# Kernel optimization log

Hardware: AMD Instinct MI355X
Metric: run time of the kernel (lower is better)

The kernel has to match this reference:

```python
import jax, jax.numpy as jnp
import numpy as np

N_NODES = 50000
N_EDGES = 200000
D = 128          # in_channels == num_hidden_channels == out_channels (set_out_input_dim_equal)
H = 4            # num_att_heads
C = D            # out_channels per head
R = 8            # num_relations
NEG_SLOPE = 0.2  # GATv2 leaky_relu slope


def gelu(x):
    # torch nn.GELU default = exact erf form
    return jax.nn.gelu(x, approximate=False)


def setup_inputs() -> dict:
    key = jax.random.key(0)
    ks = jax.random.split(key, 8)
    embs = jax.random.normal(ks[0], (N_NODES, D), dtype=jnp.float32)
    edge_index = jax.random.randint(ks[1], (2, N_EDGES), 0, N_NODES)
    edge_type = jax.random.randint(ks[2], (N_EDGES,), 0, R)
    # glorot for relation matrices [R, 2D, D]
    lim = float(np.sqrt(6.0 / (2 * D + D)))
    rel_matrices = jax.random.uniform(ks[3], (R, 2 * D, D), jnp.float32, -lim, lim)
    # GATv2Conv lin_l (== lin_r, share_weights=True): D -> H*C, with bias
    lim_l = float(np.sqrt(6.0 / (D + H * C)))
    W_l = jax.random.uniform(ks[4], (D, H * C), jnp.float32, -lim_l, lim_l)
    b_l = jnp.zeros((H * C,), jnp.float32)
    # lin_edge: edge_dim=D -> H*C, no bias
    W_e = jax.random.uniform(ks[5], (D, H * C), jnp.float32, -lim_l, lim_l)
    # attention vector att: [H, C]
    lim_a = float(np.sqrt(6.0 / C))
    att = jax.random.uniform(ks[6], (H, C), jnp.float32, -lim_a, lim_a)
    # final bias (concat=True -> size H*C)
    bias = jnp.zeros((H * C,), jnp.float32)
    return {"embs": embs, "edge_index": edge_index, "edge_type": edge_type,
            "rel_matrices": rel_matrices, "W_l": W_l, "b_l": b_l,
            "W_e": W_e, "att": att, "bias": bias, "batch_size": 1024}


def reference(embs, edge_index, edge_type, rel_matrices, W_l, b_l, W_e, att, bias, batch_size):
    src = edge_index[0]  # x_j / message source
    trg = edge_index[1]  # x_i / aggregation target

    # ---- create_edge_attrs: per-edge relation-specific bmm + GELU ----
    e_emb = jnp.concatenate([embs[src], embs[trg]], axis=1)  # [E, 2D]
    acc = jnp.zeros((e_emb.shape[0], D), e_emb.dtype)
    for r in range(R):  # fixed small relation set; avoids [E,2D,D] materialization
        acc = acc + jnp.where((edge_type == r)[:, None], e_emb @ rel_matrices[r], 0.0)
    edge_attr = gelu(acc)  # [E, D]

    # ---- GATv2Conv (share_weights=True, add_self_loops=False, concat) ----
    x = (embs @ W_l + b_l).reshape(N_NODES, H, C)  # lin_l == lin_r
    x_j = x[src]                                    # [E, H, C]
    x_i = x[trg]                                    # [E, H, C]
    e_p = (edge_attr @ W_e).reshape(-1, H, C)       # [E, H, C]

    z = jax.nn.leaky_relu(x_i + x_j + e_p, NEG_SLOPE)
    logits = jnp.einsum('ehc,hc->eh', z, att)       # [E, H]

    # edge softmax over incoming edges per target node (numerically stable)
    m = jax.ops.segment_max(logits, trg, num_segments=N_NODES)
    m = jnp.where(jnp.isfinite(m), m, 0.0)
    ex = jnp.exp(logits - m[trg])
    s = jax.ops.segment_sum(ex, trg, num_segments=N_NODES)
    alpha = ex / jnp.maximum(s[trg], 1e-16)         # [E, H]

    out = jax.ops.segment_sum(x_j * alpha[..., None], trg, num_segments=N_NODES)
    out = out.reshape(N_NODES, H * C) + bias        # concat heads
    # single (last) layer: no trailing dropout / GELU
    return out
```

## Files before the change

kernel.cpp:

```cpp
#include <hip/hip_runtime.h>
#include <math.h>

#define D_DIM 128
#define TWO_D 256
#define HC    512
#define NH    4
#define RNUM  8
#define BM    128

#define M_CNT  0
#define M_OFF  8
#define M_BLK  17
#define M_CUR  26
#define M_CUR2 34

typedef __attribute__((ext_vector_type(8))) short v8s;
typedef __attribute__((ext_vector_type(4))) float v4f;
typedef __attribute__((ext_vector_type(8))) unsigned short us8;

#define MFMA(a,b,c) __builtin_amdgcn_mfma_f32_16x16x32_bf16((a),(b),(c),0,0,0)

__device__ __forceinline__ float bf2f(unsigned short v){
    return __uint_as_float(((unsigned)v) << 16);
}
__device__ __forceinline__ unsigned short f2bf(float f){
    unsigned u = __float_as_uint(f);
    u += 0x7fffu + ((u >> 16) & 1u);
    return (unsigned short)(u >> 16);
}

__device__ __forceinline__ v8s frag_ld(const unsigned short* buf, int r, int chunk){
    return *(const v8s*)(buf + r * 64 + ((chunk ^ (r & 7)) << 3));
}

template<typename RowFn>
__device__ __forceinline__ void stage_gl(unsigned short* lds, RowFn rowp, int col0, int tid){
    const int lane = tid & 63;
    const int w = tid >> 6;
    #pragma unroll
    for (int i = 0; i < 4; i++){
        const int k = w * 4 + i;
        const int o = k * 1024 + lane * 16;
        const int rr = o >> 7;
        const int cp = (o & 127) >> 4;
        const int cg = cp ^ (rr & 7);
        const unsigned short* src = rowp(rr) + col0 + cg * 8;
        unsigned short* dst = lds + k * 512;
        __builtin_amdgcn_global_load_lds((const __attribute__((address_space(1))) void*)src,
                                         (__attribute__((address_space(3))) void*)dst,
                                         16, 0, 0);
    }
}

__global__ void k_prep(const float* __restrict__ embs, const float* __restrict__ rel,
                       const float* __restrict__ W_e, const float* __restrict__ W_l,
                       unsigned short* __restrict__ embs_bf, unsigned short* __restrict__ rel_t,
                       unsigned short* __restrict__ W_e_t, unsigned short* __restrict__ W_l_t,
                       int* __restrict__ meta, int* __restrict__ tcnt, int* __restrict__ tcur,
                       int N){
    const long T0 = (long)N * D_DIM;
    const long T1 = T0 + (long)RNUM * D_DIM * TWO_D;
    const long T2 = T1 + (long)HC * D_DIM;
    const long T3 = T2 + (long)HC * D_DIM;
    const long stride = (long)gridDim.x * blockDim.x;
    const long gid = (long)blockIdx.x * blockDim.x + threadIdx.x;

    for (long i = gid; i < N; i += stride){ tcnt[i] = 0; tcur[i] = 0; }
    if (gid < RNUM) meta[M_CNT + gid] = 0;

    const long NE8 = T0 / 8;
    for (long i = gid; i < NE8; i += stride){
        const float4* p = (const float4*)(embs + i * 8);
        float4 a = p[0], b = p[1];
        us8 o;
        o[0]=f2bf(a.x); o[1]=f2bf(a.y); o[2]=f2bf(a.z); o[3]=f2bf(a.w);
        o[4]=f2bf(b.x); o[5]=f2bf(b.y); o[6]=f2bf(b.z); o[7]=f2bf(b.w);
        *(us8*)(embs_bf + i * 8) = o;
    }
    for (long i = T0 + gid; i < T3; i += stride){
        if (i < T1){
            long j = i - T0;
            int r = (int)(j >> 15);
            int rem = (int)(j & 32767);
            int n = rem >> 8, k = rem & 255;
            rel_t[j] = f2bf(rel[(long)r * 32768 + (long)k * D_DIM + n]);
        } else if (i < T2){
            long j = i - T1;
            int n = (int)(j >> 7), k = (int)(j & 127);
            W_e_t[j] = f2bf(W_e[(long)k * HC + n]);
        } else {
            long j = i - T2;
            int n = (int)(j >> 7), k = (int)(j & 127);
            W_l_t[j] = f2bf(W_l[(long)k * HC + n]);
        }
    }
}

__global__ void k_count(const int* __restrict__ etype, const int* __restrict__ trg,
                        int* __restrict__ meta, int* __restrict__ tcnt, int E){
    __shared__ int h[RNUM];
    int tid = threadIdx.x;
    if (tid < RNUM) h[tid] = 0;
    __syncthreads();
    int e = blockIdx.x * 256 + tid;
    if (e < E){
        atomicAdd(&h[etype[e]], 1);
        atomicAdd(&tcnt[trg[e]], 1);
    }
    __syncthreads();
    if (tid < RNUM) atomicAdd(&meta[M_CNT + tid], h[tid]);
}

__global__ __launch_bounds__(256) void k_bsum(const int* __restrict__ tcnt,
                                              int* __restrict__ bsum,
                                              int* __restrict__ meta, int N){
    __shared__ int red[256];
    int tid = threadIdx.x;
    int i = blockIdx.x * 256 + tid;
    red[tid] = (i < N) ? tcnt[i] : 0;
    __syncthreads();
    for (int off = 128; off > 0; off >>= 1){
        if (tid < off) red[tid] += red[tid + off];
        __syncthreads();
    }
    if (tid == 0) bsum[blockIdx.x] = red[0];
    if (blockIdx.x == 0 && tid == 0){
        int offv = 0, blkv = 0;
        meta[M_OFF] = 0; meta[M_BLK] = 0;
        for (int r2 = 0; r2 < RNUM; r2++){
            int c = meta[M_CNT + r2];
            offv += c; blkv += (c + BM - 1) / BM;
            meta[M_OFF + r2 + 1] = offv;
            meta[M_BLK + r2 + 1] = blkv;
            meta[M_CUR + r2] = 0;
            meta[M_CUR2 + r2] = 0;
        }
    }
}

__global__ __launch_bounds__(256) void k_cscan(const int* __restrict__ tcnt,
                                               const int* __restrict__ bsum,
                                               int* __restrict__ rowptr, int N, int NB){
    __shared__ int pre[256];
    __shared__ int sOff;
    int tid = threadIdx.x;
    int b = blockIdx.x;

    int s = 0;
    for (int j = tid; j < b; j += 256) s += bsum[j];
    pre[tid] = s;
    __syncthreads();
    for (int off = 128; off > 0; off >>= 1){
        if (tid < off) pre[tid] += pre[tid + off];
        __syncthreads();
    }
    if (tid == 0) sOff = pre[0];
    __syncthreads();
    const int base = sOff;
    __syncthreads();

    int i = b * 256 + tid;
    int v = (i < N) ? tcnt[i] : 0;
    pre[tid] = v;
    __syncthreads();
    for (int off = 1; off < 256; off <<= 1){
        int t = (tid >= off) ? pre[tid - off] : 0;
        __syncthreads();
        pre[tid] += t;
        __syncthreads();
    }
    if (i < N) rowptr[i] = base + pre[tid] - v;
    if (i == N) rowptr[N] = base + pre[tid];
    if (b == NB - 1 && (b + 1) * 256 == N && tid == 255)
        rowptr[N] = base + pre[255];
}

__global__ void k_scatter2(const int* __restrict__ etype, const int* __restrict__ trg,
                           const int* __restrict__ src,
                           const int* __restrict__ rowptr, int* __restrict__ tcur,
                           int* __restrict__ srcp, int* __restrict__ trgp,
                           int* __restrict__ etypep, int E){
    int e = blockIdx.x * 256 + threadIdx.x;
    if (e < E){
        int t = trg[e];
        int pos = rowptr[t] + atomicAdd(&tcur[t], 1);
        srcp[pos] = src[e];
        trgp[pos] = t;
        etypep[pos] = etype[e];
    }
}

__global__ void k_rscatter(const int* __restrict__ etypep, int* __restrict__ meta,
                           int* __restrict__ perm, int E){
    __shared__ int lcnt[RNUM], lbase[RNUM];
    int tid = threadIdx.x;
    if (tid < RNUM) lcnt[tid] = 0;
    __syncthreads();
    int p = blockIdx.x * 256 + tid;
    int r = 0, rank = 0;
    if (p < E){ r = etypep[p]; rank = atomicAdd(&lcnt[r], 1); }
    __syncthreads();
    if (tid < RNUM) lbase[tid] = atomicAdd(&meta[M_CUR2 + tid], lcnt[tid]);
    __syncthreads();
    if (p < E) perm[meta[M_OFF + r] + lbase[r] + rank] = p;
}

#define ZP 132

__global__ __launch_bounds__(256, 4) void k_x_mfma(
    const unsigned short* __restrict__ embs_bf, const unsigned short* __restrict__ W_l_t,
    const float* __restrict__ b_l, unsigned short* __restrict__ x_bf, int N)
{
    __shared__ __align__(16) char smem[64 * ZP * 4];
    unsigned short* Ab = (unsigned short*)smem;
    unsigned short* Bb = (unsigned short*)(smem + 16384);
    float* zb = (float*)smem;

    const int tid = threadIdx.x;
    const int n0 = blockIdx.x * BM;
    const int cg = blockIdx.y;
    const int cnt = min(BM, N - n0);
    const int w = tid >> 6, lane = tid & 63, m = lane & 15, q = lane >> 4;

    v4f acc[2][8];
    #pragma unroll
    for (int i = 0; i < 2; i++)
        #pragma unroll
        for (int j = 0; j < 8; j++) acc[i][j] = 0.f;

    #pragma unroll
    for (int ch = 0; ch < 2; ch++){
        __syncthreads();
        stage_gl(Ab, [&](int rr){ return embs_bf + (long)min(n0 + rr, N - 1) * D_DIM; },
                 ch * 64, tid);
        stage_gl(Bb, [&](int rr){ return W_l_t + (long)(cg * BM + rr) * D_DIM; },
                 ch * 64, tid);
        __syncthreads();
        #pragma unroll
        for (int ks = 0; ks < 2; ks++){
            v8s af[2], bf[8];
            #pragma unroll
            for (int rt = 0; rt < 2; rt++) af[rt] = frag_ld(Ab, w*32 + rt*16 + m, ks*4 + q);
            #pragma unroll
            for (int ct = 0; ct < 8; ct++) bf[ct] = frag_ld(Bb, ct*16 + m, ks*4 + q);
            #pragma unroll
            for (int rt = 0; rt < 2; rt++)
                #pragma unroll
                for (int ct = 0; ct < 8; ct++)
                    acc[rt][ct] = MFMA(af[rt], bf[ct], acc[rt][ct]);
        }
    }
    __syncthreads();

    for (int pp = 0; pp < 2; pp++){
        if ((w >> 1) == pp){
            int wr = (w & 1) * 32;
            #pragma unroll
            for (int rt = 0; rt < 2; rt++)
                #pragma unroll
                for (int ct = 0; ct < 8; ct++)
                    #pragma unroll
                    for (int g = 0; g < 4; g++)
                        zb[(wr + rt*16 + q*4 + g) * ZP + ct*16 + m] = acc[rt][ct][g];
        }
        __syncthreads();
        int rl = tid >> 2, pq = tid & 3;
        int row = pp * 64 + rl;
        if (row < cnt){
            const float* zp = zb + rl * ZP + pq * 32;
            const float* blp = b_l + cg * BM + pq * 32;
            long dst = (long)(n0 + row) * HC + cg * BM + pq * 32;
            #pragma unroll
            for (int g2 = 0; g2 < 4; g2++){
                us8 o;
                #pragma unroll
                for (int j = 0; j < 8; j++)
                    o[j] = f2bf(zp[g2*8 + j] + blp[g2*8 + j]);
                *(us8*)&x_bf[dst + g2*8] = o;
            }
        }
        __syncthreads();
    }
}

__global__ __launch_bounds__(256, 4) void k_attr_mfma(
    const unsigned short* __restrict__ embs_bf, const int* __restrict__ srcp,
    const int* __restrict__ trgp, const unsigned short* __restrict__ rel_t,
    const int* __restrict__ perm, const int* __restrict__ meta,
    unsigned short* __restrict__ edge_attrp)
{
    __shared__ __align__(16) char smem[64 * ZP * 4];
    unsigned short* Ab = (unsigned short*)smem;
    unsigned short* Bb = (unsigned short*)(smem + 16384);
    float* zb = (float*)smem;
    __shared__ int s_ep[BM], s_s[BM], s_t[BM];
    __shared__ int s_meta[3];

    const int tid = threadIdx.x;
    const int b = blockIdx.x;
    if (tid == 0){
        int nblk = meta[M_BLK + RNUM];
        if (b >= nblk){ s_meta[0] = -1; }
        else {
            int r = 0;
            while (b >= meta[M_BLK + r + 1]) r++;
            int chunk = b - meta[M_BLK + r];
            int base = meta[M_OFF + r] + chunk * BM;
            s_meta[0] = r; s_meta[1] = base;
            s_meta[2] = min(BM, meta[M_OFF + r + 1] - base);
        }
    }
    __syncthreads();
    const int r = s_meta[0];
    if (r < 0) return;
    const int base = s_meta[1], cnt = s_meta[2];
    if (tid < BM){
        int pos = perm[base + min(tid, cnt - 1)];
        s_ep[tid] = pos; s_s[tid] = srcp[pos]; s_t[tid] = trgp[pos];
    }
    const int w = tid >> 6, lane = tid & 63, m = lane & 15, q = lane >> 4;

    v4f acc[2][8];
    #pragma unroll
    for (int i = 0; i < 2; i++)
        #pragma unroll
        for (int j = 0; j < 8; j++) acc[i][j] = 0.f;

    __syncthreads();

    #pragma unroll
    for (int ch = 0; ch < 4; ch++){
        __syncthreads();
        stage_gl(Ab, [&](int rr){ int node = (ch < 2) ? s_s[rr] : s_t[rr];
                                  return embs_bf + (long)node * D_DIM; },
                 (ch & 1) * 64, tid);
        stage_gl(Bb, [&](int rr){ return rel_t + ((long)r * BM + rr) * TWO_D; },
                 ch * 64, tid);
        __syncthreads();
        #pragma unroll
        for (int ks = 0; ks < 2; ks++){
            v8s af[2], bf[8];
            #pragma unroll
            for (int rt = 0; rt < 2; rt++) af[rt] = frag_ld(Ab, w*32 + rt*16 + m, ks*4 + q);
            #pragma unroll
            for (int ct = 0; ct < 8; ct++) bf[ct] = frag_ld(Bb, ct*16 + m, ks*4 + q);
            #pragma unroll
            for (int rt = 0; rt < 2; rt++)
                #pragma unroll
                for (int ct = 0; ct < 8; ct++)
                    acc[rt][ct] = MFMA(af[rt], bf[ct], acc[rt][ct]);
        }
    }
    __syncthreads();

    for (int pp = 0; pp < 2; pp++){
        if ((w >> 1) == pp){
            int wr = (w & 1) * 32;
            #pragma unroll
            for (int rt = 0; rt < 2; rt++)
                #pragma unroll
                for (int ct = 0; ct < 8; ct++)
                    #pragma unroll
                    for (int g = 0; g < 4; g++)
                        zb[(wr + rt*16 + q*4 + g) * ZP + ct*16 + m] = acc[rt][ct][g];
        }
        __syncthreads();
        int rl = tid >> 2, pq = tid & 3;
        int row = pp * 64 + rl;
        if (row < cnt){
            const float* zp = zb + rl * ZP + pq * 32;
            long dst = (long)s_ep[row] * D_DIM + pq * 32;
            #pragma unroll
            for (int g2 = 0; g2 < 4; g2++){
                us8 o;
                #pragma unroll
                for (int j = 0; j < 8; j++){
                    float v = zp[g2*8 + j];
                    v = 0.5f * v * (1.f + erff(v * 0.70710678118654752f));
                    o[j] = f2bf(v);
                }
                *(us8*)&edge_attrp[dst + g2*8] = o;
            }
        }
        __syncthreads();
    }
}

__global__ __launch_bounds__(256, 4) void k_logits_mfma(
    const unsigned short* __restrict__ edge_attrp, const unsigned short* __restrict__ W_e_t,
    const float* __restrict__ att, const unsigned short* __restrict__ x_bf,
    const int* __restrict__ srcp, const int* __restrict__ trgp,
    float* __restrict__ logitsp, int E)
{
    __shared__ __align__(16) char smem[64 * ZP * 4];
    unsigned short* Ab = (unsigned short*)smem;
    unsigned short* Bb = (unsigned short*)(smem + 16384);
    float* zb = (float*)smem;
    __shared__ int s_s[BM], s_t[BM];

    const int tid = threadIdx.x;
    const int bid = blockIdx.x;
    const int g = bid >> 5, r5 = bid & 31;
    const int tile = g * 8 + (r5 & 7);
    const int h = r5 >> 3;
    const int lbv = (E + BM - 1) / BM;
    if (tile >= lbv) return;
    const int e0 = tile * BM;
    const int cnt = min(BM, E - e0);
    if (tid < BM){
        int e = e0 + min(tid, cnt - 1);
        s_s[tid] = srcp[e]; s_t[tid] = trgp[e];
    }
    const int w = tid >> 6, lane = tid & 63, m = lane & 15, q = lane >> 4;

    v4f acc[2][8];
    #pragma unroll
    for (int i = 0; i < 2; i++)
        #pragma unroll
        for (int j = 0; j < 8; j++) acc[i][j] = 0.f;

    #pragma unroll
    for (int ch = 0; ch < 2; ch++){
        __syncthreads();
        stage_gl(Ab, [&](int rr){ return edge_attrp + (long)(e0 + min(rr, cnt - 1)) * D_DIM; },
                 ch * 64, tid);
        stage_gl(Bb, [&](int rr){ return W_e_t + (long)(h * BM + rr) * D_DIM; },
                 ch * 64, tid);
        __syncthreads();
        #pragma unroll
        for (int ks = 0; ks < 2; ks++){
            v8s af[2], bf[8];
            #pragma unroll
            for (int rt = 0; rt < 2; rt++) af[rt] = frag_ld(Ab, w*32 + rt*16 + m, ks*4 + q);
            #pragma unroll
            for (int ct = 0; ct < 8; ct++) bf[ct] = frag_ld(Bb, ct*16 + m, ks*4 + q);
            #pragma unroll
            for (int rt = 0; rt < 2; rt++)
                #pragma unroll
                for (int ct = 0; ct < 8; ct++)
                    acc[rt][ct] = MFMA(af[rt], bf[ct], acc[rt][ct]);
        }
    }
    __syncthreads();

    for (int pp = 0; pp < 2; pp++){
        if ((w >> 1) == pp){
            int wr = (w & 1) * 32;
            #pragma unroll
            for (int rt = 0; rt < 2; rt++)
                #pragma unroll
                for (int ct = 0; ct < 8; ct++)
                    #pragma unroll
                    for (int g2 = 0; g2 < 4; g2++)
                        zb[(wr + rt*16 + q*4 + g2) * ZP + ct*16 + m] = acc[rt][ct][g2];
        }
        __syncthreads();
        int rl = tid >> 2, pq = tid & 3;
        int row = pp * 64 + rl;
        float part = 0.f;
        if (row < cnt){
            int s = s_s[row], t = s_t[row];
            const float* zp = zb + rl * ZP + pq * 32;
            const unsigned short* xip = x_bf + (long)t * HC + h * BM + pq * 32;
            const unsigned short* xjp = x_bf + (long)s * HC + h * BM + pq * 32;
            const float* ap = att + h * BM + pq * 32;
            #pragma unroll
            for (int g2 = 0; g2 < 4; g2++){
                us8 xi = *(const us8*)(xip + g2*8);
                us8 xj = *(const us8*)(xjp + g2*8);
                #pragma unroll
                for (int j = 0; j < 8; j++){
                    float z = zp[g2*8 + j] + bf2f(xi[j]) + bf2f(xj[j]);
                    z = (z > 0.f) ? z : 0.2f * z;
                    part += z * ap[g2*8 + j];
                }
            }
        }
        part += __shfl_xor(part, 1, 64);
        part += __shfl_xor(part, 2, 64);
        if ((tid & 3) == 0 && row < cnt)
            logitsp[(long)(e0 + row) * NH + h] = part;
        __syncthreads();
    }
}

__global__ __launch_bounds__(256) void k_agg_csr(
    const float* __restrict__ logitsp, const int* __restrict__ rowptr,
    const int* __restrict__ srcp,
    const unsigned short* __restrict__ x_bf, const float* __restrict__ bias,
    float* __restrict__ out, int N)
{
    int t = blockIdx.x * 4 + (threadIdx.x >> 6);
    if (t >= N) return;
    int lane = threadIdx.x & 63;
    int c0 = lane * 8;
    int h = lane >> 4;
    int lo = rowptr[t], hi = rowptr[t + 1];

    float acc[8];
    #pragma unroll
    for (int j = 0; j < 8; j++) acc[j] = 0.f;

    if (lo < hi){
        float mx = -3.0e38f;
        for (int i = lo; i < hi; i++)
            mx = fmaxf(mx, logitsp[(long)i * NH + h]);
        float ssum = 0.f;
        for (int i = lo; i < hi; i++){
            float ew = expf(logitsp[(long)i * NH + h] - mx);
            ssum += ew;
            us8 xv = *(const us8*)&x_bf[(long)srcp[i] * HC + c0];
            #pragma unroll
            for (int j = 0; j < 8; j++) acc[j] += ew * bf2f(xv[j]);
        }
        float inv = 1.f / fmaxf(ssum, 1e-16f);
        #pragma unroll
        for (int j = 0; j < 8; j++) acc[j] *= inv;
    }
    long dst = (long)t * HC + c0;
    *(float4*)&out[dst]     = make_float4(acc[0] + bias[c0+0], acc[1] + bias[c0+1],
                                          acc[2] + bias[c0+2], acc[3] + bias[c0+3]);
    *(float4*)&out[dst + 4] = make_float4(acc[4] + bias[c0+4], acc[5] + bias[c0+5],
                                          acc[6] + bias[c0+6], acc[7] + bias[c0+7]);
}

extern "C" void kernel_launch(void* const* d_in, const int* in_sizes, int n_in,
                              void* d_out, int out_size, void* d_ws, size_t ws_size,
                              hipStream_t stream) {
    const float* embs       = (const float*)d_in[0];
    const int*   edge_index = (const int*)  d_in[1];
    const int*   etype      = (const int*)  d_in[2];
    const float* rel        = (const float*)d_in[3];
    const float* W_l        = (const float*)d_in[4];
    const float* b_l        = (const float*)d_in[5];
    const float* W_e        = (const float*)d_in[6];
    const float* att        = (const float*)d_in[7];
    const float* bias       = (const float*)d_in[8];

    const int N = in_sizes[0] / D_DIM;
    const int E = in_sizes[1] / 2;
    const int* src = edge_index;
    const int* trg = edge_index + E;

    char* ws = (char*)d_ws;
    size_t off = 0;
    unsigned short* x_bf = (unsigned short*)(ws + off);      off += (size_t)N * HC * 2;
    unsigned short* embs_bf = (unsigned short*)(ws + off);   off += (size_t)N * D_DIM * 2;
    unsigned short* edge_attrp = (unsigned short*)(ws + off); off += (size_t)E * D_DIM * 2;
    unsigned short* rel_t = (unsigned short*)(ws + off);     off += (size_t)RNUM * D_DIM * TWO_D * 2;
    unsigned short* W_e_t = (unsigned short*)(ws + off);     off += (size_t)HC * D_DIM * 2;
    unsigned short* W_l_t = (unsigned short*)(ws + off);     off += (size_t)HC * D_DIM * 2;
    float* logitsp = (float*)(ws + off);                     off += (size_t)E * NH * 4;
    int* perm = (int*)(ws + off);                            off += (size_t)E * 4;
    int* meta = (int*)(ws + off);                            off += 64 * 4;
    int* tcnt = (int*)(ws + off);                            off += (size_t)N * 4;
    int* tcur = (int*)(ws + off);                            off += (size_t)N * 4;
    int* rowptr = (int*)(ws + off);                          off += (size_t)(N + 1) * 4;
    int* etypep = (int*)(ws + off);                          off += (size_t)E * 4;
    int* srcp = (int*)(ws + off);                            off += (size_t)E * 4;
    int* trgp = (int*)(ws + off);                            off += (size_t)E * 4;
    int* bsum = (int*)(ws + off);                            off += 1024 * 4;

    float* out = (float*)d_out;

    const int eb = (E + 255) / 256;
    const int nb = (N + 255) / 256;
    const int ab = (E + BM - 1) / BM + RNUM;
    const int lb = (E + BM - 1) / BM;
    const int lgrid = ((lb + 7) / 8) * 32;

    k_prep<<<2048, 256, 0, stream>>>(embs, rel, W_e, W_l, embs_bf, rel_t, W_e_t, W_l_t,
                                     meta, tcnt, tcur, N);
    k_count<<<eb, 256, 0, stream>>>(etype, trg, meta, tcnt, E);
    k_bsum<<<nb, 256, 0, stream>>>(tcnt, bsum, meta, N);
    k_cscan<<<nb, 256, 0, stream>>>(tcnt, bsum, rowptr, N, nb);
    k_scatter2<<<eb, 256, 0, stream>>>(etype, trg, src, rowptr, tcur, srcp, trgp, etypep, E);
    k_rscatter<<<eb, 256, 0, stream>>>(etypep, meta, perm, E);
    k_x_mfma<<<dim3((N + BM - 1) / BM, NH), 256, 0, stream>>>(embs_bf, W_l_t, b_l, x_bf, N);
    k_attr_mfma<<<ab, 256, 0, stream>>>(embs_bf, srcp, trgp, rel_t, perm, meta, edge_attrp);
    k_logits_mfma<<<lgrid, 256, 0, stream>>>(edge_attrp, W_e_t, att, x_bf, srcp, trgp,
                                             logitsp, E);
    k_agg_csr<<<(N + 3) / 4, 256, 0, stream>>>(logitsp, rowptr, srcp, x_bf, bias, out, N);
}
```

Baseline: 397.9 us.

## Recompute x_i + x_j inside logits GEMM by accumulating gathered embeddings times W_l

The logits kernel no longer gathers precomputed bf16 x rows for source and target. It extends the K loop from 2 to 6 chunks, accumulating embs[src]@W_l and embs[trg]@W_l into the same MFMA accumulator as edge_attr@W_e, and adds 2*b_l in the epilogue. This removes the per-edge gathers of x_bf and the rounding of x to bf16, but triples the MFMA work and staging traffic per tile. The loop is no longer unrolled. x_bf is still computed because aggregation uses it.

```diff
diff --git a/kernel.cpp b/kernel.cpp
--- a/kernel.cpp
+++ b/kernel.cpp
@@ -386,9 +386,10 @@
     }
 }
 
-__global__ __launch_bounds__(256, 4) void k_logits_mfma(
-    const unsigned short* __restrict__ edge_attrp, const unsigned short* __restrict__ W_e_t,
-    const float* __restrict__ att, const unsigned short* __restrict__ x_bf,
+__global__ __launch_bounds__(256, 4) void k_logits_fused(
+    const unsigned short* __restrict__ edge_attrp, const unsigned short* __restrict__ embs_bf,
+    const unsigned short* __restrict__ W_e_t, const unsigned short* __restrict__ W_l_t,
+    const float* __restrict__ b_l, const float* __restrict__ att,
     const int* __restrict__ srcp, const int* __restrict__ trgp,
     float* __restrict__ logitsp, int E)
 {
@@ -419,13 +420,23 @@
         #pragma unroll
         for (int j = 0; j < 8; j++) acc[i][j] = 0.f;
 
-    #pragma unroll
-    for (int ch = 0; ch < 2; ch++){
-        __syncthreads();
-        stage_gl(Ab, [&](int rr){ return edge_attrp + (long)(e0 + min(rr, cnt - 1)) * D_DIM; },
-                 ch * 64, tid);
-        stage_gl(Bb, [&](int rr){ return W_e_t + (long)(h * BM + rr) * D_DIM; },
-                 ch * 64, tid);
+    __syncthreads();
+
+    #pragma unroll 1
+    for (int ch = 0; ch < 6; ch++){
+        __syncthreads();
+        if (ch < 2)
+            stage_gl(Ab, [&](int rr){ return edge_attrp + (long)(e0 + min(rr, cnt - 1)) * D_DIM; },
+                     (ch & 1) * 64, tid);
+        else if (ch < 4)
+            stage_gl(Ab, [&](int rr){ return embs_bf + (long)s_s[rr] * D_DIM; },
+                     (ch & 1) * 64, tid);
+        else
+            stage_gl(Ab, [&](int rr){ return embs_bf + (long)s_t[rr] * D_DIM; },
+                     (ch & 1) * 64, tid);
+        const unsigned short* Wb = (ch < 2) ? W_e_t : W_l_t;
+        stage_gl(Bb, [&](int rr){ return Wb + (long)(h * BM + rr) * D_DIM; },
+                 (ch & 1) * 64, tid);
         __syncthreads();
         #pragma unroll
         for (int ks = 0; ks < 2; ks++){
@@ -459,19 +470,15 @@
         int row = pp * 64 + rl;
         float part = 0.f;
         if (row < cnt){
-            int s = s_s[row], t = s_t[row];
             const float* zp = zb + rl * ZP + pq * 32;
-            const unsigned short* xip = x_bf + (long)t * HC + h * BM + pq * 32;
-            const unsigned short* xjp = x_bf + (long)s * HC + h * BM + pq * 32;
             const float* ap = att + h * BM + pq * 32;
+            const float* blp = b_l + h * BM + pq * 32;
             #pragma unroll
             for (int g2 = 0; g2 < 4; g2++){
-                us8 xi = *(const us8*)(xip + g2*8);
-                us8 xj = *(const us8*)(xjp + g2*8);
                 #pragma unroll
                 for (int j = 0; j < 8; j++){
-                    float z = zp[g2*8 + j] + bf2f(xi[j]) + bf2f(xj[j]);
-                    z = (z > 0.f) ? z : 0.2f * z;
+                    float z = zp[g2*8 + j] + 2.0f * blp[g2*8 + j];
+                    z = fmaxf(z, 0.2f * z);
                     part += z * ap[g2*8 + j];
                 }
             }
@@ -578,7 +585,7 @@
     k_rscatter<<<eb, 256, 0, stream>>>(etypep, meta, perm, E);
     k_x_mfma<<<dim3((N + BM - 1) / BM, NH), 256, 0, stream>>>(embs_bf, W_l_t, b_l, x_bf, N);
     k_attr_mfma<<<ab, 256, 0, stream>>>(embs_bf, srcp, trgp, rel_t, perm, meta, edge_attrp);
-    k_logits_mfma<<<lgrid, 256, 0, stream>>>(edge_attrp, W_e_t, att, x_bf, srcp, trgp,
-                                             logitsp, E);
+    k_logits_fused<<<lgrid, 256, 0, stream>>>(edge_attrp, embs_bf, W_e_t, W_l_t, b_l, att,
+                                              srcp, trgp, logitsp, E);
     k_agg_csr<<<(N + 3) / 4, 256, 0, stream>>>(logitsp, rowptr, srcp, x_bf, bias, out, N);
 }
```

Measured after the change: 485.8 us. 22.1% more time.
